# Kernel optimization log

Measured on AMD Instinct MI355X. Metric: run time of the kernel, lower is better.

## Reference

```python
import jax, jax.numpy as jnp
import numpy as np

B = 262144      # batch of states (PPO rollout)
J = 16          # num_pools -> state_dim=32, action_dim=256
M = 12          # num_epochs_per_day (experts)
H = 34          # hidden_dim (fixed in source)
A = J * J


def setup_inputs() -> dict:
    key = jax.random.key(0)
    ks = jax.random.split(key, 6)
    states = jax.random.normal(ks[0], (B, 2 * J), dtype=jnp.float32)
    epoch_idx = jax.random.randint(ks[1], (B,), 0, M, dtype=jnp.int32)
    # fc1: kaiming normal (relu), zero bias
    W1 = jax.random.normal(ks[2], (H, 2 * J), dtype=jnp.float32) * np.sqrt(2.0 / (2 * J))
    b1 = jnp.zeros((H,), dtype=jnp.float32)
    # m expert output layers [M, A, H]
    Wout = jax.random.normal(ks[3], (M, A, H), dtype=jnp.float32) * np.sqrt(1.0 / H)
    bout = jax.random.normal(ks[4], (M, A), dtype=jnp.float32) * np.sqrt(1.0 / H)
    mask = jax.random.randint(ks[5], (J, J), 0, 2, dtype=jnp.int32)
    return {"states": states, "epoch_idx": epoch_idx, "W1": W1, "b1": b1,
            "Wout": Wout, "bout": bout, "mask": mask}


def reference(states, epoch_idx, W1, b1, Wout, bout, mask):
    # shared trunk: [B, H]
    x = jax.nn.relu(jnp.einsum('bs,hs->bh', states, W1) + b1)
    # grouped expert GEMM via one-hot routing (equivalent to output_layers[epoch_idx])
    onehot = jax.nn.one_hot(epoch_idx, M, dtype=x.dtype)           # [B, M]
    xe = x[:, None, :] * onehot[:, :, None]                        # [B, M, H]
    logits = jnp.einsum('bmh,mah->ba', xe, Wout) + bout[epoch_idx]  # [B, A]
    logits = logits.reshape(-1, J, J)
    NEG = jnp.float32(-1e9)
    return jnp.where(mask == 0, NEG, logits)
```

## Files before the change

### kernel.cpp

```cpp
#include <hip/hip_runtime.h>

typedef __attribute__((ext_vector_type(8))) short short8;
typedef __attribute__((ext_vector_type(4))) float f32x4;
typedef __attribute__((ext_vector_type(4))) int   i32x4;

#define SDIM 32
#define HDIM 34
#define NEXP 12
#define ACOL 256
#define SPB  256
#define MAXROWS 448
#define STG_STRIDE 260

#define BAR_RAW()  asm volatile("s_barrier" ::: "memory")
#define BAR_LGKM() asm volatile("s_waitcnt lgkmcnt(0)\n\ts_barrier" ::: "memory")

__device__ __forceinline__ unsigned int bpack(float lo, float hi) {
    unsigned int a = __builtin_bit_cast(unsigned int, lo);
    unsigned int b = __builtin_bit_cast(unsigned int, hi);
    return ((a + 0x8000u) >> 16) | ((b + 0x8000u) & 0xffff0000u);
}

__global__ __launch_bounds__(256, 3) void actor_kernel(
    const float* __restrict__ states,
    const int*   __restrict__ epoch_idx,
    const float* __restrict__ W1,
    const float* __restrict__ b1,
    const float* __restrict__ Wout,
    const float* __restrict__ bout,
    const int*   __restrict__ mask,
    float*       __restrict__ out,
    int nB)
{
    __shared__ __align__(16) unsigned int xs[MAXROWS * 16];
    __shared__ unsigned int   xt[MAXROWS];
    __shared__ unsigned short rowid[MAXROWS];
    __shared__ __align__(16) float stg[16 * STG_STRIDE];
    __shared__ int cnt[NEXP], goff[NEXP], ntl[NEXP];

    float* w1s = stg;
    float* b1s = stg + HDIM * SDIM;

    const int t  = threadIdx.x;
    const int s0 = blockIdx.x * SPB;

    for (int i = t; i < HDIM * SDIM; i += 256) w1s[i] = W1[i];
    if (t < HDIM) b1s[t] = b1[t];
    if (t < NEXP) cnt[t] = 0;
    for (int i = t; i < MAXROWS; i += 256) rowid[i] = 0xFFFFu;

    const int  sidx  = s0 + t;
    const bool valid = (sidx < nB);
    float sr[SDIM];
    int e = 0;
    if (valid) {
        const f32x4* sp = (const f32x4*)(states + (size_t)sidx * SDIM);
        #pragma unroll
        for (int q = 0; q < SDIM / 4; ++q) {
            f32x4 v = sp[q];
            sr[4*q+0] = v[0]; sr[4*q+1] = v[1]; sr[4*q+2] = v[2]; sr[4*q+3] = v[3];
        }
        e = epoch_idx[sidx];
    }
    __syncthreads();

    int rank = 0;
    if (valid) rank = atomicAdd(&cnt[e], 1);
    __syncthreads();

    if (t == 0) {
        int base = 0;
        #pragma unroll
        for (int i = 0; i < NEXP; ++i) {
            goff[i] = base;
            int nt = (cnt[i] + 15) >> 4;
            ntl[i] = nt;
            base += nt << 4;
        }
    }
    float x[HDIM];
    if (valid) {
        #pragma unroll 2
        for (int h = 0; h < HDIM; ++h) {
            float acc = b1s[h];
            const float4* wr = (const float4*)(w1s + h * SDIM);
            #pragma unroll
            for (int q = 0; q < SDIM / 4; ++q) {
                float4 wv = wr[q];
                acc = fmaf(sr[4*q+0], wv.x, acc);
                acc = fmaf(sr[4*q+1], wv.y, acc);
                acc = fmaf(sr[4*q+2], wv.z, acc);
                acc = fmaf(sr[4*q+3], wv.w, acc);
            }
            x[h] = fmaxf(acc, 0.0f);
        }
    }
    __syncthreads();

    if (valid) {
        const int slot = goff[e] + rank;
        const unsigned sw = (((unsigned)slot >> 2) & 3u) << 4;
        char* rbase = (char*)xs + slot * 64;
        unsigned d[16];
        #pragma unroll
        for (int k = 0; k < 16; ++k) d[k] = bpack(x[2*k], x[2*k+1]);
        #pragma unroll
        for (int c = 0; c < 4; ++c) {
            f32x4 q;
            q[0] = __builtin_bit_cast(float, d[4*c+0]);
            q[1] = __builtin_bit_cast(float, d[4*c+1]);
            q[2] = __builtin_bit_cast(float, d[4*c+2]);
            q[3] = __builtin_bit_cast(float, d[4*c+3]);
            *(f32x4*)(rbase + (((unsigned)(c * 16)) ^ sw)) = q;
        }
        xt[slot]    = bpack(x[32], x[33]);
        rowid[slot] = (unsigned short)t;
    }
    __syncthreads();

    const int wv   = t >> 6;
    const int lane = t & 63;
    const int r    = lane & 15;
    const int g    = lane >> 4;
    const int colbase = wv * 64 + r;
    const float NEG = -1e9f;
    const i32x4 mq = *(const i32x4*)(mask + 4 * lane);

    float* outb = out + (size_t)s0 * ACOL;

    for (int e2 = 0; e2 < NEXP; ++e2) {
        const int ntiles = ntl[e2];
        if (ntiles == 0) continue;

        short8   bf1[4];
        unsigned w2[4];
        float    bias[4];
        #pragma unroll
        for (int j = 0; j < 4; ++j) {
            const int col = colbase + j * 16;
            const float* wr = Wout + ((size_t)e2 * ACOL + col) * HDIM;
            const float2* wp = (const float2*)(wr + g * 8);
            float2 p0 = wp[0], p1 = wp[1], p2 = wp[2], p3 = wp[3];
            uint4 q1 = make_uint4(bpack(p0.x, p0.y), bpack(p1.x, p1.y),
                                  bpack(p2.x, p2.y), bpack(p3.x, p3.y));
            bf1[j] = __builtin_bit_cast(short8, q1);
            w2[j]  = (g == 0) ? bpack(wr[32], wr[33]) : 0u;
            bias[j] = bout[e2 * ACOL + col];
        }

        const int tb = goff[e2];
        for (int st = 0; st < ntiles; ++st) {
            const int rb  = tb + (st << 4);
            const int row = rb + r;
            const unsigned sw = (((unsigned)row >> 2) & 3u) << 4;
            const char* rp = (const char*)xs + row * 64;
            short8 a1 = *(const short8*)(rp + (((unsigned)(g * 16)) ^ sw));
            short8 a2 = __builtin_bit_cast(short8,
                          make_uint4(g == 0 ? xt[row] : 0u, 0u, 0u, 0u));

            f32x4 acc[4];
            #pragma unroll
            for (int j = 0; j < 4; ++j) {
                f32x4 a = {bias[j], bias[j], bias[j], bias[j]};
                a = __builtin_amdgcn_mfma_f32_16x16x32_bf16(a1, bf1[j], a, 0, 0, 0);
                short8 b2 = __builtin_bit_cast(short8,
                              make_uint4(w2[j], 0u, 0u, 0u));
                a = __builtin_amdgcn_mfma_f32_16x16x32_bf16(a2, b2, a, 0, 0, 0);
                acc[j] = a;
            }

            BAR_RAW();
            #pragma unroll
            for (int j = 0; j < 4; ++j) {
                const int c = colbase + 16 * j;
                #pragma unroll
                for (int i = 0; i < 4; ++i)
                    stg[(g * 4 + i) * STG_STRIDE + c] = acc[j][i];
            }
            BAR_LGKM();

            #pragma unroll
            for (int q = 0; q < 4; ++q) {
                const int lrow = wv * 4 + q;
                const unsigned rid = rowid[rb + lrow];
                f32x4 v = *(const f32x4*)&stg[lrow * STG_STRIDE + 4 * lane];
                v[0] = mq[0] ? v[0] : NEG;
                v[1] = mq[1] ? v[1] : NEG;
                v[2] = mq[2] ? v[2] : NEG;
                v[3] = mq[3] ? v[3] : NEG;
                if (rid != 0xFFFFu)
                    __builtin_nontemporal_store(v,
                        (f32x4*)(outb + (size_t)rid * ACOL + 4 * lane));
            }
        }
    }
}

extern "C" void kernel_launch(void* const* d_in, const int* in_sizes, int n_in,
                              void* d_out, int out_size, void* d_ws, size_t ws_size,
                              hipStream_t stream) {
    const float* states    = (const float*)d_in[0];
    const int*   epoch_idx = (const int*)  d_in[1];
    const float* W1        = (const float*)d_in[2];
    const float* b1        = (const float*)d_in[3];
    const float* Wout      = (const float*)d_in[4];
    const float* bout      = (const float*)d_in[5];
    const int*   mask      = (const int*)  d_in[6];
    float*       out       = (float*)d_out;

    const int nB   = in_sizes[0] / SDIM;
    const int grid = (nB + SPB - 1) / SPB;
    actor_kernel<<<grid, 256, 0, stream>>>(states, epoch_idx, W1, b1,
                                           Wout, bout, mask, out, nB);
}
```

Measured before the change: 101.1 us.

## Split row tiles across wave pairs with per-wave staging to drop block barriers

```diff
diff --git a/kernel.cpp b/kernel.cpp
--- a/kernel.cpp
+++ b/kernel.cpp
@@ -2,7 +2,7 @@
 
 typedef __attribute__((ext_vector_type(8))) short short8;
 typedef __attribute__((ext_vector_type(4))) float f32x4;
-typedef __attribute__((ext_vector_type(4))) int   i32x4;
+typedef __attribute__((ext_vector_type(2))) float f32x2;
 
 #define SDIM 32
 #define HDIM 34
@@ -10,10 +10,7 @@
 #define ACOL 256
 #define SPB  256
 #define MAXROWS 448
-#define STG_STRIDE 260
-
-#define BAR_RAW()  asm volatile("s_barrier" ::: "memory")
-#define BAR_LGKM() asm volatile("s_waitcnt lgkmcnt(0)\n\ts_barrier" ::: "memory")
+#define STGS 132
 
 __device__ __forceinline__ unsigned int bpack(float lo, float hi) {
     unsigned int a = __builtin_bit_cast(unsigned int, lo);
@@ -21,7 +18,7 @@
     return ((a + 0x8000u) >> 16) | ((b + 0x8000u) & 0xffff0000u);
 }
 
-__global__ __launch_bounds__(256, 3) void actor_kernel(
+__global__ __launch_bounds__(256, 2) void actor_kernel(
     const float* __restrict__ states,
     const int*   __restrict__ epoch_idx,
     const float* __restrict__ W1,
@@ -35,11 +32,11 @@
     __shared__ __align__(16) unsigned int xs[MAXROWS * 16];
     __shared__ unsigned int   xt[MAXROWS];
     __shared__ unsigned short rowid[MAXROWS];
-    __shared__ __align__(16) float stg[16 * STG_STRIDE];
+    __shared__ __align__(16) float stg[4][16 * STGS];
     __shared__ int cnt[NEXP], goff[NEXP], ntl[NEXP];
 
-    float* w1s = stg;
-    float* b1s = stg + HDIM * SDIM;
+    float* w1s = &stg[0][0];
+    float* b1s = w1s + HDIM * SDIM;
 
     const int t  = threadIdx.x;
     const int s0 = blockIdx.x * SPB;
@@ -120,11 +117,15 @@
 
     const int wv   = t >> 6;
     const int lane = t & 63;
+    const int p    = wv >> 1;
+    const int qh   = wv & 1;
     const int r    = lane & 15;
     const int g    = lane >> 4;
-    const int colbase = wv * 64 + r;
+    const int hb   = qh * 128;
+    float* mystg   = stg[wv];
     const float NEG = -1e9f;
-    const i32x4 mq = *(const i32x4*)(mask + 4 * lane);
+    const int m0 = mask[hb + 2 * lane];
+    const int m1 = mask[hb + 2 * lane + 1];
 
     float* outb = out + (size_t)s0 * ACOL;
 
@@ -132,12 +133,12 @@
         const int ntiles = ntl[e2];
         if (ntiles == 0) continue;
 
-        short8   bf1[4];
-        unsigned w2[4];
-        float    bias[4];
-        #pragma unroll
-        for (int j = 0; j < 4; ++j) {
-            const int col = colbase + j * 16;
+        short8   bf1[8];
+        unsigned w2[8];
+        float    bias[8];
+        #pragma unroll
+        for (int j = 0; j < 8; ++j) {
+            const int col = hb + j * 16 + r;
             const float* wr = Wout + ((size_t)e2 * ACOL + col) * HDIM;
             const float2* wp = (const float2*)(wr + g * 8);
             float2 p0 = wp[0], p1 = wp[1], p2 = wp[2], p3 = wp[3];
@@ -148,8 +149,10 @@
             bias[j] = bout[e2 * ACOL + col];
         }
 
-        const int tb = goff[e2];
+        const int tb  = goff[e2];
+        const int gt0 = tb >> 4;
         for (int st = 0; st < ntiles; ++st) {
+            if (((gt0 + st) & 1) != p) continue;
             const int rb  = tb + (st << 4);
             const int row = rb + r;
             const unsigned sw = (((unsigned)row >> 2) & 3u) << 4;
@@ -158,39 +161,26 @@
             short8 a2 = __builtin_bit_cast(short8,
                           make_uint4(g == 0 ? xt[row] : 0u, 0u, 0u, 0u));
 
-            f32x4 acc[4];
             #pragma unroll
-            for (int j = 0; j < 4; ++j) {
+            for (int j = 0; j < 8; ++j) {
                 f32x4 a = {bias[j], bias[j], bias[j], bias[j]};
                 a = __builtin_amdgcn_mfma_f32_16x16x32_bf16(a1, bf1[j], a, 0, 0, 0);
                 short8 b2 = __builtin_bit_cast(short8,
                               make_uint4(w2[j], 0u, 0u, 0u));
                 a = __builtin_amdgcn_mfma_f32_16x16x32_bf16(a2, b2, a, 0, 0, 0);
-                acc[j] = a;
-            }
-
-            BAR_RAW();
-            #pragma unroll
-            for (int j = 0; j < 4; ++j) {
-                const int c = colbase + 16 * j;
                 #pragma unroll
                 for (int i = 0; i < 4; ++i)
-                    stg[(g * 4 + i) * STG_STRIDE + c] = acc[j][i];
+                    mystg[(4 * g + i) * STGS + 16 * j + r] = a[i];
             }
-            BAR_LGKM();
-
             #pragma unroll
-            for (int q = 0; q < 4; ++q) {
-                const int lrow = wv * 4 + q;
+            for (int lrow = 0; lrow < 16; ++lrow) {
                 const unsigned rid = rowid[rb + lrow];
-                f32x4 v = *(const f32x4*)&stg[lrow * STG_STRIDE + 4 * lane];
-                v[0] = mq[0] ? v[0] : NEG;
-                v[1] = mq[1] ? v[1] : NEG;
-                v[2] = mq[2] ? v[2] : NEG;
-                v[3] = mq[3] ? v[3] : NEG;
+                f32x2 v = *(const f32x2*)&mystg[lrow * STGS + 2 * lane];
+                v[0] = m0 ? v[0] : NEG;
+                v[1] = m1 ? v[1] : NEG;
                 if (rid != 0xFFFFu)
                     __builtin_nontemporal_store(v,
-                        (f32x4*)(outb + (size_t)rid * ACOL + 4 * lane));
+                        (f32x2*)(outb + (size_t)rid * ACOL + hb + 2 * lane));
             }
         }
     }
```

Result: slower. 122.2 us (+20.9%).

## Prepack expert weights to bf16 and double-buffer the output staging tile

Applied to the files above, without the earlier changes.

```diff
diff --git a/kernel.cpp b/kernel.cpp
--- a/kernel.cpp
+++ b/kernel.cpp
@@ -12,7 +12,6 @@
 #define MAXROWS 448
 #define STG_STRIDE 260
 
-#define BAR_RAW()  asm volatile("s_barrier" ::: "memory")
 #define BAR_LGKM() asm volatile("s_waitcnt lgkmcnt(0)\n\ts_barrier" ::: "memory")
 
 __device__ __forceinline__ unsigned int bpack(float lo, float hi) {
@@ -21,12 +20,38 @@
     return ((a + 0x8000u) >> 16) | ((b + 0x8000u) & 0xffff0000u);
 }
 
-__global__ __launch_bounds__(256, 3) void actor_kernel(
+__global__ __launch_bounds__(256) void k0_wpack(
+    const float* __restrict__ Wout, uint4* __restrict__ wpack,
+    unsigned int* __restrict__ w2p)
+{
+    const int tid = blockIdx.x * 256 + threadIdx.x;
+    if (tid >= NEXP * 4 * 4 * 64) return;
+    const int lane = tid & 63;
+    const int j    = (tid >> 6) & 3;
+    const int wvv  = (tid >> 8) & 3;
+    const int e    = tid >> 10;
+    const int r = lane & 15, g = lane >> 4;
+    const int col = wvv * 64 + j * 16 + r;
+    const float* wr = Wout + ((size_t)e * ACOL + col) * HDIM;
+    uint4 q;
+    q.x = bpack(wr[g*8+0], wr[g*8+1]);
+    q.y = bpack(wr[g*8+2], wr[g*8+3]);
+    q.z = bpack(wr[g*8+4], wr[g*8+5]);
+    q.w = bpack(wr[g*8+6], wr[g*8+7]);
+    wpack[tid] = q;
+    if (tid < NEXP * ACOL) {
+        const float* wr2 = Wout + (size_t)tid * HDIM;
+        w2p[tid] = bpack(wr2[32], wr2[33]);
+    }
+}
+
+__global__ __launch_bounds__(256, 2) void actor_kernel(
     const float* __restrict__ states,
     const int*   __restrict__ epoch_idx,
     const float* __restrict__ W1,
     const float* __restrict__ b1,
-    const float* __restrict__ Wout,
+    const uint4* __restrict__ wpack,
+    const unsigned int* __restrict__ w2p,
     const float* __restrict__ bout,
     const int*   __restrict__ mask,
     float*       __restrict__ out,
@@ -35,11 +60,11 @@
     __shared__ __align__(16) unsigned int xs[MAXROWS * 16];
     __shared__ unsigned int   xt[MAXROWS];
     __shared__ unsigned short rowid[MAXROWS];
-    __shared__ __align__(16) float stg[16 * STG_STRIDE];
+    __shared__ __align__(16) float stg[2][16 * STG_STRIDE];
     __shared__ int cnt[NEXP], goff[NEXP], ntl[NEXP];
 
-    float* w1s = stg;
-    float* b1s = stg + HDIM * SDIM;
+    float* w1s = &stg[0][0];
+    float* b1s = w1s + HDIM * SDIM;
 
     const int t  = threadIdx.x;
     const int s0 = blockIdx.x * SPB;
@@ -127,6 +152,7 @@
     const i32x4 mq = *(const i32x4*)(mask + 4 * lane);
 
     float* outb = out + (size_t)s0 * ACOL;
+    int buf = 0;
 
     for (int e2 = 0; e2 < NEXP; ++e2) {
         const int ntiles = ntl[e2];
@@ -135,17 +161,12 @@
         short8   bf1[4];
         unsigned w2[4];
         float    bias[4];
+        const uint4* wp = wpack + ((size_t)(e2 * 4 + wv) * 4) * 64 + lane;
         #pragma unroll
         for (int j = 0; j < 4; ++j) {
-            const int col = colbase + j * 16;
-            const float* wr = Wout + ((size_t)e2 * ACOL + col) * HDIM;
-            const float2* wp = (const float2*)(wr + g * 8);
-            float2 p0 = wp[0], p1 = wp[1], p2 = wp[2], p3 = wp[3];
-            uint4 q1 = make_uint4(bpack(p0.x, p0.y), bpack(p1.x, p1.y),
-                                  bpack(p2.x, p2.y), bpack(p3.x, p3.y));
-            bf1[j] = __builtin_bit_cast(short8, q1);
-            w2[j]  = (g == 0) ? bpack(wr[32], wr[33]) : 0u;
-            bias[j] = bout[e2 * ACOL + col];
+            bf1[j]  = __builtin_bit_cast(short8, wp[j * 64]);
+            w2[j]   = (g == 0) ? w2p[e2 * ACOL + colbase + j * 16] : 0u;
+            bias[j] = bout[e2 * ACOL + colbase + j * 16];
         }
 
         const int tb = goff[e2];
@@ -158,7 +179,6 @@
             short8 a2 = __builtin_bit_cast(short8,
                           make_uint4(g == 0 ? xt[row] : 0u, 0u, 0u, 0u));
 
-            f32x4 acc[4];
             #pragma unroll
             for (int j = 0; j < 4; ++j) {
                 f32x4 a = {bias[j], bias[j], bias[j], bias[j]};
@@ -166,32 +186,33 @@
                 short8 b2 = __builtin_bit_cast(short8,
                               make_uint4(w2[j], 0u, 0u, 0u));
                 a = __builtin_amdgcn_mfma_f32_16x16x32_bf16(a2, b2, a, 0, 0, 0);
-                acc[j] = a;
-            }
-
-            BAR_RAW();
-            #pragma unroll
-            for (int j = 0; j < 4; ++j) {
                 const int c = colbase + 16 * j;
                 #pragma unroll
                 for (int i = 0; i < 4; ++i)
-                    stg[(g * 4 + i) * STG_STRIDE + c] = acc[j][i];
-            }
+                    stg[buf][(g * 4 + i) * STG_STRIDE + c] = a[i];
+            }
+
             BAR_LGKM();
 
+            f32x4 v[4];
+            unsigned rid[4];
             #pragma unroll
             for (int q = 0; q < 4; ++q) {
                 const int lrow = wv * 4 + q;
-                const unsigned rid = rowid[rb + lrow];
-                f32x4 v = *(const f32x4*)&stg[lrow * STG_STRIDE + 4 * lane];
-                v[0] = mq[0] ? v[0] : NEG;
-                v[1] = mq[1] ? v[1] : NEG;
-                v[2] = mq[2] ? v[2] : NEG;
-                v[3] = mq[3] ? v[3] : NEG;
-                if (rid != 0xFFFFu)
-                    __builtin_nontemporal_store(v,
-                        (f32x4*)(outb + (size_t)rid * ACOL + 4 * lane));
-            }
+                rid[q] = rowid[rb + lrow];
+                v[q]   = *(const f32x4*)&stg[buf][lrow * STG_STRIDE + 4 * lane];
+            }
+            #pragma unroll
+            for (int q = 0; q < 4; ++q) {
+                f32x4 w = v[q];
+                w[0] = mq[0] ? w[0] : NEG;
+                w[1] = mq[1] ? w[1] : NEG;
+                w[2] = mq[2] ? w[2] : NEG;
+                w[3] = mq[3] ? w[3] : NEG;
+                if (rid[q] != 0xFFFFu)
+                    *(f32x4*)(outb + (size_t)rid[q] * ACOL + 4 * lane) = w;
+            }
+            buf ^= 1;
         }
     }
 }
@@ -210,6 +231,11 @@
 
     const int nB   = in_sizes[0] / SDIM;
     const int grid = (nB + SPB - 1) / SPB;
+
+    uint4*        wpack = (uint4*)d_ws;
+    unsigned int* w2p   = (unsigned int*)((char*)d_ws + 196608);
+
+    k0_wpack<<<48, 256, 0, stream>>>(Wout, wpack, w2p);
     actor_kernel<<<grid, 256, 0, stream>>>(states, epoch_idx, W1, b1,
-                                           Wout, bout, mask, out, nB);
-}
+                                           wpack, w2p, bout, mask, out, nB);
+}
```

Measured after the change: 87.38 us. 13.5% less time.
